# Optimization experiments

Hardware: AMD Instinct MI355X
Metric: run time of the kernel (lower is better)

The kernel has to match this reference:

```python
import jax, jax.numpy as jnp
import numpy as np

N_NODES = 50000
N_EDGES = 800000
IN_FEATS = 64
HID_FEATS = 64


def _sage_conv(x, src, dst, W_self, W_neigh, b):
    # mean aggregation over in-neighbors (messages flow src -> dst)
    msg_sum = jax.ops.segment_sum(x[src], dst, num_segments=N_NODES)  # [N, d]
    deg = jax.ops.segment_sum(jnp.ones((src.shape[0],), x.dtype), dst,
                              num_segments=N_NODES)  # [N]
    h_neigh = msg_sum / jnp.maximum(deg, 1.0)[:, None]  # zero-degree nodes -> 0
    return x @ W_self + h_neigh @ W_neigh + b


def setup_inputs() -> dict:
    key = jax.random.key(0)
    ks = jax.random.split(key, 12)
    inputs = jax.random.normal(ks[0], (N_NODES, IN_FEATS), dtype=jnp.float32)
    src = jax.random.randint(ks[1], (N_EDGES,), 0, N_NODES, dtype=jnp.int32)
    dst = jax.random.randint(ks[2], (N_EDGES,), 0, N_NODES, dtype=jnp.int32)

    def glorot(k, shape):
        lim = float(np.sqrt(6.0 / (shape[0] + shape[1])))
        return jax.random.uniform(k, shape, jnp.float32, -lim, lim)

    return {
        "inputs": inputs, "src": src, "dst": dst,
        "W_self1": glorot(ks[3], (IN_FEATS, HID_FEATS)),
        "W_neigh1": glorot(ks[4], (IN_FEATS, HID_FEATS)),
        "b1": jnp.zeros((HID_FEATS,), jnp.float32),
        "W_self2": glorot(ks[5], (HID_FEATS, HID_FEATS)),
        "W_neigh2": glorot(ks[6], (HID_FEATS, HID_FEATS)),
        "b2": jnp.zeros((HID_FEATS,), jnp.float32),
        "W_self3": glorot(ks[7], (HID_FEATS, 1)),
        "W_neigh3": glorot(ks[8], (HID_FEATS, 1)),
        "b3": jnp.zeros((1,), jnp.float32),
    }


def reference(inputs, src, dst,
              W_self1, W_neigh1, b1,
              W_self2, W_neigh2, b2,
              W_self3, W_neigh3, b3):
    h = jax.nn.relu(_sage_conv(inputs, src, dst, W_self1, W_neigh1, b1))
    h = jax.nn.relu(_sage_conv(h, src, dst, W_self2, W_neigh2, b2))
    h = _sage_conv(h, src, dst, W_self3, W_neigh3, b3)
    return h  # [N_NODES, 1]
```

## Files before the change

### kernel.cpp

```cpp
#include <hip/hip_runtime.h>

#define N_NODES 50000
#define N_EDGES 800000
#define F 64
#define NTILES (N_NODES / 16)

#define BNODES 128
#define NB ((N_NODES + BNODES - 1) / BNODES)
#define BCAP 2560
#define EPB 3200
#define SCAT_BLOCKS (N_EDGES / EPB)
#define PREP_ELEMS (4 * F * F + N_NODES * 16)
#define PREP_BLOCKS ((PREP_ELEMS + 511) / 512)

typedef __attribute__((ext_vector_type(8))) short short8;
typedef __attribute__((ext_vector_type(4))) float f32x4;

union frag16 { uint4 u; short8 s; };


__device__ __forceinline__ float bflo(unsigned int u) {
    union { unsigned int i; float f; } c; c.i = u << 16; return c.f;
}
__device__ __forceinline__ float bfhi(unsigned int u) {
    union { unsigned int i; float f; } c; c.i = u & 0xFFFF0000u; return c.f;
}
__device__ __forceinline__ unsigned short f2bf(float f) {
    union { float f; unsigned int i; } c; c.f = f;
    unsigned int r = c.i + 0x7FFF + ((c.i >> 16) & 1);
    return (unsigned short)(r >> 16);
}


__global__ __launch_bounds__(512) void scatter_prep(
        const int* __restrict__ src, const int* __restrict__ dst,
        int* __restrict__ bcur, unsigned int* __restrict__ binned,
        const float* __restrict__ W0, const float* __restrict__ W1,
        const float* __restrict__ W2, const float* __restrict__ W3,
        unsigned short* __restrict__ Wt,
        const float4* __restrict__ xin, ushort4* __restrict__ xout) {
    if (blockIdx.x >= SCAT_BLOCKS) {
        int idx = (blockIdx.x - SCAT_BLOCKS) * 512 + threadIdx.x;
        if (idx < 4 * F * F) {
            int m = idx >> 12;
            int e = idx & 4095;
            int n = e >> 6, k = e & 63;
            const float* W = (m == 0) ? W0 : (m == 1) ? W1 : (m == 2) ? W2 : W3;
            Wt[m * F * F + n * F + k] = f2bf(W[k * F + n]);
            return;
        }
        int i = idx - 4 * F * F;
        if (i >= N_NODES * 16) return;
        float4 v = xin[i];
        ushort4 o;
        o.x = f2bf(v.x); o.y = f2bf(v.y); o.z = f2bf(v.z); o.w = f2bf(v.w);
        xout[i] = o;
        return;
    }

    __shared__ int lcnt[NB];
    __shared__ int scan[512];
    __shared__ int gbase[NB];
    __shared__ int lcur[NB];
    __shared__ unsigned int staged[EPB];
    int tid = threadIdx.x;
    int e0 = blockIdx.x * EPB;
    int e1 = min(N_EDGES, e0 + EPB);
    for (int i = tid; i < NB; i += 512) lcnt[i] = 0;
    __syncthreads();
    for (int i = e0 + tid; i < e1; i += 512)
        atomicAdd(&lcnt[dst[i] >> 7], 1);
    __syncthreads();
    int v = (tid < NB) ? lcnt[tid] : 0;
    scan[tid] = v;
    __syncthreads();
    for (int off = 1; off < 512; off <<= 1) {
        int t = (tid >= off) ? scan[tid - off] : 0;
        __syncthreads();
        scan[tid] += t;
        __syncthreads();
    }
    if (tid < NB) {
        int excl = scan[tid] - v;
        int resv = (v > 0) ? atomicAdd(&bcur[tid], v) : 0;
        gbase[tid] = tid * BCAP + resv - excl;
        lcur[tid] = excl;
    }
    __syncthreads();
    for (int i = e0 + tid; i < e1; i += 512) {
        int d = dst[i];
        int b = d >> 7;
        int dl = d & 127;
        int posl = atomicAdd(&lcur[b], 1);
        staged[posl] = (unsigned)src[i] | ((unsigned)dl << 16) | ((unsigned)b << 23);
    }
    __syncthreads();
    int cnt = e1 - e0;
    for (int i = tid; i < cnt; i += 512) {
        unsigned pk = staged[i];
        int b = pk >> 23;
        binned[gbase[b] + i] = pk;
    }
}


__global__ __launch_bounds__(256) void bucket_build(const unsigned int* __restrict__ binned,
                                                    const int* __restrict__ bcur,
                                                    int* __restrict__ row_beg,
                                                    unsigned short* __restrict__ degs,
                                                    unsigned short* __restrict__ csr16) {
    int b = blockIdx.x;
    int start = b * BCAP;
    int cnt = bcur[b];
    __shared__ int ncnt[BNODES];
    __shared__ int nofs[BNODES];
    __shared__ int ncur[BNODES];
    int tid = threadIdx.x;
    for (int i = tid; i < BNODES; i += 256) ncnt[i] = 0;
    __syncthreads();
    for (int i = tid; i < cnt; i += 256)
        atomicAdd(&ncnt[(binned[start + i] >> 16) & 127], 1);
    __syncthreads();
    if (tid < 128) nofs[tid] = ncnt[tid];
    __syncthreads();
    for (int off = 1; off < 128; off <<= 1) {
        int t = (tid >= off && tid < 128) ? nofs[tid - off] : 0;
        __syncthreads();
        if (tid < 128) nofs[tid] += t;
        __syncthreads();
    }
    if (tid < 128) {
        int excl = nofs[tid] - ncnt[tid];
        ncur[tid] = excl;
        int node = b * BNODES + tid;
        row_beg[node] = start + excl;
        degs[node] = (unsigned short)ncnt[tid];
    }
    __syncthreads();
    for (int i = tid; i < cnt; i += 256) {
        unsigned pk = binned[start + i];
        int dl = (pk >> 16) & 127;
        int pos = start + atomicAdd(&ncur[dl], 1);
        csr16[pos] = (unsigned short)(pk & 0xFFFF);
    }
}


__global__ __launch_bounds__(256) void aggregate_kernel(
        const uint4* __restrict__ xh8, const int* __restrict__ row_beg,
        const unsigned short* __restrict__ degs,
        const unsigned short* __restrict__ csr16, uint4* __restrict__ aggh8, int n_nodes) {
    int wave = threadIdx.x >> 6;
    int lane = threadIdx.x & 63;
    int node = blockIdx.x * 4 + wave;
    if (node >= n_nodes) return;
    int g   = lane >> 3;
    int sub = lane & 7;
    int beg = row_beg[node];
    int deg = degs[node];
    int end = beg + deg;
    float a0[8], a1[8];
    #pragma unroll
    for (int j = 0; j < 8; ++j) { a0[j] = 0.f; a1[j] = 0.f; }
    int i = beg + g;
    for (; i + 8 < end; i += 16) {
        int i0 = csr16[i];
        int i1 = csr16[i + 8];
        uint4 v0 = xh8[i0 * 8 + sub];
        uint4 v1 = xh8[i1 * 8 + sub];
        a0[0] += bflo(v0.x); a0[1] += bfhi(v0.x); a0[2] += bflo(v0.y); a0[3] += bfhi(v0.y);
        a0[4] += bflo(v0.z); a0[5] += bfhi(v0.z); a0[6] += bflo(v0.w); a0[7] += bfhi(v0.w);
        a1[0] += bflo(v1.x); a1[1] += bfhi(v1.x); a1[2] += bflo(v1.y); a1[3] += bfhi(v1.y);
        a1[4] += bflo(v1.z); a1[5] += bfhi(v1.z); a1[6] += bflo(v1.w); a1[7] += bfhi(v1.w);
    }
    if (i < end) {
        uint4 v0 = xh8[csr16[i] * 8 + sub];
        a0[0] += bflo(v0.x); a0[1] += bfhi(v0.x); a0[2] += bflo(v0.y); a0[3] += bfhi(v0.y);
        a0[4] += bflo(v0.z); a0[5] += bfhi(v0.z); a0[6] += bflo(v0.w); a0[7] += bfhi(v0.w);
    }
    float s[8];
    #pragma unroll
    for (int j = 0; j < 8; ++j) s[j] = a0[j] + a1[j];
    #pragma unroll
    for (int off = 8; off <= 32; off <<= 1)
        #pragma unroll
        for (int j = 0; j < 8; ++j)
            s[j] += __shfl_xor(s[j], off);
    if (g == 0) {
        float inv = (deg > 0) ? (1.0f / (float)deg) : 0.f;
        unsigned short o[8];
        #pragma unroll
        for (int j = 0; j < 8; ++j) o[j] = f2bf(s[j] * inv);
        uint4 pk;
        pk.x = (unsigned)o[0] | ((unsigned)o[1] << 16);
        pk.y = (unsigned)o[2] | ((unsigned)o[3] << 16);
        pk.z = (unsigned)o[4] | ((unsigned)o[5] << 16);
        pk.w = (unsigned)o[6] | ((unsigned)o[7] << 16);
        aggh8[node * 8 + sub] = pk;
    }
}


__global__ __launch_bounds__(256) void mfma_transform(
        const uint4* __restrict__ xh, const uint4* __restrict__ aggh,
        const uint4* __restrict__ Wst, const uint4* __restrict__ Wnt,
        const float* __restrict__ b,
        unsigned short* __restrict__ out_bf,
        const float* __restrict__ Ws3, const float* __restrict__ Wn3,
        float* __restrict__ pout, float* __restrict__ qout, int ntiles) {
    int wv   = threadIdx.x >> 6;
    int lane = threadIdx.x & 63;
    int tile = blockIdx.x * 4 + wv;
    if (tile >= ntiles) return;
    int lo = lane & 15, hi = lane >> 4;

    frag16 ws[2][4], wn[2][4];
    #pragma unroll
    for (int kt = 0; kt < 2; ++kt)
        #pragma unroll
        for (int jt = 0; jt < 4; ++jt) {
            int n = jt * 16 + lo;
            ws[kt][jt].u = Wst[n * 8 + kt * 4 + hi];
            wn[kt][jt].u = Wnt[n * 8 + kt * 4 + hi];
        }

    float bias_s[4];
    #pragma unroll
    for (int jt = 0; jt < 4; ++jt) bias_s[jt] = b[jt * 16 + lo];
    float w3n_s[4], w3s_s[4];
    if (pout) {
        #pragma unroll
        for (int jt = 0; jt < 4; ++jt) {
            w3n_s[jt] = Wn3[jt * 16 + lo];
            w3s_s[jt] = Ws3[jt * 16 + lo];
        }
    }

    int base = tile * 16;
    int node = base + lo;

    frag16 ax[2], aa[2];
    #pragma unroll
    for (int kt = 0; kt < 2; ++kt) {
        ax[kt].u = xh[node * 8 + kt * 4 + hi];
        aa[kt].u = aggh[node * 8 + kt * 4 + hi];
    }

    f32x4 acc[4];
    #pragma unroll
    for (int jt = 0; jt < 4; ++jt)
        acc[jt] = f32x4{bias_s[jt], bias_s[jt], bias_s[jt], bias_s[jt]};

    #pragma unroll
    for (int kt = 0; kt < 2; ++kt)
        #pragma unroll
        for (int jt = 0; jt < 4; ++jt) {
            acc[jt] = __builtin_amdgcn_mfma_f32_16x16x32_bf16(ax[kt].s, ws[kt][jt].s, acc[jt], 0, 0, 0);
            acc[jt] = __builtin_amdgcn_mfma_f32_16x16x32_bf16(aa[kt].s, wn[kt][jt].s, acc[jt], 0, 0, 0);
        }

    if (out_bf) {
        #pragma unroll
        for (int jt = 0; jt < 4; ++jt)
            #pragma unroll
            for (int r = 0; r < 4; ++r) {
                float h = fmaxf(acc[jt][r], 0.f);
                out_bf[(base + hi * 4 + r) * F + jt * 16 + lo] = f2bf(h);
            }
    } else {
        #pragma unroll
        for (int r = 0; r < 4; ++r) {
            float pr = 0.f, qr = 0.f;
            #pragma unroll
            for (int jt = 0; jt < 4; ++jt) {
                float h = fmaxf(acc[jt][r], 0.f);
                pr += h * w3n_s[jt];
                qr += h * w3s_s[jt];
            }
            #pragma unroll
            for (int off = 1; off < 16; off <<= 1) {
                pr += __shfl_xor(pr, off);
                qr += __shfl_xor(qr, off);
            }
            if (lo == 0) {
                pout[base + hi * 4 + r] = pr;
                qout[base + hi * 4 + r] = qr;
            }
        }
    }
}


__global__ __launch_bounds__(256) void final_kernel(
        const int* __restrict__ row_beg, const unsigned short* __restrict__ degs,
        const unsigned short* __restrict__ csr16,
        const float* __restrict__ p, const float* __restrict__ q,
        const float* __restrict__ b3, float* __restrict__ out, int n_nodes) {
    int grp = threadIdx.x >> 4;
    int ln  = threadIdx.x & 15;
    int node = blockIdx.x * 16 + grp;
    if (node >= n_nodes) return;
    int beg = row_beg[node];
    int deg = degs[node];
    int end = beg + deg;
    float s = 0.f;
    for (int i = beg + ln; i < end; i += 16) s += p[csr16[i]];
    #pragma unroll
    for (int off = 1; off < 16; off <<= 1) s += __shfl_xor(s, off);
    if (ln == 0) {
        float inv = (deg > 0) ? (1.0f / (float)deg) : 0.f;
        out[node] = q[node] + s * inv + b3[0];
    }
}


extern "C" void kernel_launch(void* const* d_in, const int* in_sizes, int n_in,
                              void* d_out, int out_size, void* d_ws, size_t ws_size,
                              hipStream_t stream) {
    const float* x   = (const float*)d_in[0];
    const int*   src = (const int*)d_in[1];
    const int*   dst = (const int*)d_in[2];
    const float* Ws1 = (const float*)d_in[3];
    const float* Wn1 = (const float*)d_in[4];
    const float* b1  = (const float*)d_in[5];
    const float* Ws2 = (const float*)d_in[6];
    const float* Wn2 = (const float*)d_in[7];
    const float* b2  = (const float*)d_in[8];
    const float* Ws3 = (const float*)d_in[9];
    const float* Wn3 = (const float*)d_in[10];
    const float* b3  = (const float*)d_in[11];
    float* out = (float*)d_out;

    char* ws = (char*)d_ws;
    size_t cur = 0;
    auto alloc = [&](size_t bytes) -> void* {
        void* p = ws + cur;
        cur += (bytes + 255) & ~(size_t)255;
        return p;
    };

    int*            bcur     = (int*)  alloc(NB * sizeof(int));
    unsigned int*   binned   = (unsigned int*)alloc((size_t)NB * BCAP * sizeof(unsigned int));
    int*            row_beg  = (int*)  alloc((size_t)(NB * BNODES) * sizeof(int));
    unsigned short* degs     = (unsigned short*)alloc((size_t)(NB * BNODES) * sizeof(unsigned short));
    unsigned short* csr16    = (unsigned short*)alloc((size_t)NB * BCAP * sizeof(unsigned short));
    unsigned short* xh       = (unsigned short*)alloc((size_t)N_NODES * F * 2);
    unsigned short* h1h      = (unsigned short*)alloc((size_t)N_NODES * F * 2);
    unsigned short* aggh     = (unsigned short*)alloc((size_t)N_NODES * F * 2);
    unsigned short* Wt       = (unsigned short*)alloc(4 * F * F * 2);
    float*          p        = (float*)alloc(N_NODES * sizeof(float));
    float*          q        = (float*)alloc(N_NODES * sizeof(float));

    unsigned short* Wst1 = Wt;
    unsigned short* Wnt1 = Wt + F * F;
    unsigned short* Wst2 = Wt + 2 * F * F;
    unsigned short* Wnt2 = Wt + 3 * F * F;

    (void)hipMemsetAsync(bcur, 0, NB * sizeof(int), stream);
    scatter_prep<<<SCAT_BLOCKS + PREP_BLOCKS, 512, 0, stream>>>(
        src, dst, bcur, binned,
        Ws1, Wn1, Ws2, Wn2, Wt, (const float4*)x, (ushort4*)xh);
    bucket_build<<<NB, 256, 0, stream>>>(binned, bcur, row_beg, degs, csr16);

    int agg_grid = (N_NODES + 3) / 4;
    int tf_grid  = (NTILES + 3) / 4;

    aggregate_kernel<<<agg_grid, 256, 0, stream>>>(
        (const uint4*)xh, row_beg, degs, csr16, (uint4*)aggh, N_NODES);
    mfma_transform<<<tf_grid, 256, 0, stream>>>(
        (const uint4*)xh, (const uint4*)aggh, (const uint4*)Wst1, (const uint4*)Wnt1,
        b1, h1h, nullptr, nullptr, nullptr, nullptr, NTILES);
    aggregate_kernel<<<agg_grid, 256, 0, stream>>>(
        (const uint4*)h1h, row_beg, degs, csr16, (uint4*)aggh, N_NODES);
    mfma_transform<<<tf_grid, 256, 0, stream>>>(
        (const uint4*)h1h, (const uint4*)aggh, (const uint4*)Wst2, (const uint4*)Wnt2,
        b2, nullptr, Ws3, Wn3, p, q, NTILES);
    final_kernel<<<(N_NODES + 15) / 16, 256, 0, stream>>>(
        row_beg, degs, csr16, p, q, b3, out, N_NODES);
}
```

Baseline: 182.0 us.

## Fuse neighbor aggregation into MFMA transform and restructure edge scatter kernels

Merges the aggregate and MFMA transform kernels into one templated kernel: each block aggregates 16 nodes into shared memory, then one wave runs the MFMA tile. This removes the global aggh round trip and two launches. The scatter kernel now uses a fixed 512-block grid with grid-stride prep work and smaller edge chunks, and it keeps src/dst in registers instead of re-reading them. The bucket build uses 512 threads with register-held entries. The cost is that three of the four waves sit idle during the MFMA phase, and there are fewer blocks for the transform.

```diff
diff --git a/kernel.cpp b/kernel.cpp
--- a/kernel.cpp
+++ b/kernel.cpp
@@ -8,10 +8,11 @@
 #define BNODES 128
 #define NB ((N_NODES + BNODES - 1) / BNODES)
 #define BCAP 2560
-#define EPB 3200
-#define SCAT_BLOCKS (N_EDGES / EPB)
+#define EPB 2048
+#define SCHUNKS ((N_EDGES + EPB - 1) / EPB)
+#define SGRID 512
+#define SBLOCK 512
 #define PREP_ELEMS (4 * F * F + N_NODES * 16)
-#define PREP_BLOCKS ((PREP_ELEMS + 511) / 512)
 
 typedef __attribute__((ext_vector_type(8))) short short8;
 typedef __attribute__((ext_vector_type(4))) float f32x4;
@@ -32,52 +33,64 @@
 }
 
 
-__global__ __launch_bounds__(512) void scatter_prep(
+__global__ __launch_bounds__(SBLOCK) void scatter_prep(
         const int* __restrict__ src, const int* __restrict__ dst,
         int* __restrict__ bcur, unsigned int* __restrict__ binned,
         const float* __restrict__ W0, const float* __restrict__ W1,
         const float* __restrict__ W2, const float* __restrict__ W3,
         unsigned short* __restrict__ Wt,
         const float4* __restrict__ xin, ushort4* __restrict__ xout) {
-    if (blockIdx.x >= SCAT_BLOCKS) {
-        int idx = (blockIdx.x - SCAT_BLOCKS) * 512 + threadIdx.x;
+    __shared__ int lcnt[NB];
+    __shared__ int scan[SBLOCK];
+    __shared__ int gbase[NB];
+    __shared__ int lcur[NB];
+    __shared__ unsigned int staged[EPB];
+
+    int tid = threadIdx.x;
+    int blk = blockIdx.x;
+
+    for (int idx = blk * SBLOCK + tid; idx < PREP_ELEMS; idx += SGRID * SBLOCK) {
         if (idx < 4 * F * F) {
             int m = idx >> 12;
             int e = idx & 4095;
             int n = e >> 6, k = e & 63;
             const float* W = (m == 0) ? W0 : (m == 1) ? W1 : (m == 2) ? W2 : W3;
             Wt[m * F * F + n * F + k] = f2bf(W[k * F + n]);
-            return;
-        }
-        int i = idx - 4 * F * F;
-        if (i >= N_NODES * 16) return;
-        float4 v = xin[i];
-        ushort4 o;
-        o.x = f2bf(v.x); o.y = f2bf(v.y); o.z = f2bf(v.z); o.w = f2bf(v.w);
-        xout[i] = o;
-        return;
-    }
-
-    __shared__ int lcnt[NB];
-    __shared__ int scan[512];
-    __shared__ int gbase[NB];
-    __shared__ int lcur[NB];
-    __shared__ unsigned int staged[EPB];
-    int tid = threadIdx.x;
-    int e0 = blockIdx.x * EPB;
+        } else {
+            int i = idx - 4 * F * F;
+            float4 v = xin[i];
+            ushort4 o;
+            o.x = f2bf(v.x); o.y = f2bf(v.y); o.z = f2bf(v.z); o.w = f2bf(v.w);
+            xout[i] = o;
+        }
+    }
+
+    if (blk >= SCHUNKS) return;
+
+    int e0 = blk * EPB;
     int e1 = min(N_EDGES, e0 + EPB);
-    for (int i = tid; i < NB; i += 512) lcnt[i] = 0;
-    __syncthreads();
-    for (int i = e0 + tid; i < e1; i += 512)
-        atomicAdd(&lcnt[dst[i] >> 7], 1);
-    __syncthreads();
+    for (int i = tid; i < NB; i += SBLOCK) lcnt[i] = 0;
+    __syncthreads();
+
+    int dreg[4], sreg[4];
+    #pragma unroll
+    for (int t = 0; t < 4; ++t) {
+        int i = e0 + tid + t * SBLOCK;
+        if (i < e1) { dreg[t] = dst[i]; sreg[t] = src[i]; }
+        else        { dreg[t] = -1;     sreg[t] = 0; }
+    }
+    #pragma unroll
+    for (int t = 0; t < 4; ++t)
+        if (dreg[t] >= 0) atomicAdd(&lcnt[dreg[t] >> 7], 1);
+    __syncthreads();
+
     int v = (tid < NB) ? lcnt[tid] : 0;
     scan[tid] = v;
     __syncthreads();
-    for (int off = 1; off < 512; off <<= 1) {
-        int t = (tid >= off) ? scan[tid - off] : 0;
+    for (int off = 1; off < SBLOCK; off <<= 1) {
+        int t2 = (tid >= off) ? scan[tid - off] : 0;
         __syncthreads();
-        scan[tid] += t;
+        scan[tid] += t2;
         __syncthreads();
     }
     if (tid < NB) {
@@ -87,131 +100,151 @@
         lcur[tid] = excl;
     }
     __syncthreads();
-    for (int i = e0 + tid; i < e1; i += 512) {
-        int d = dst[i];
-        int b = d >> 7;
-        int dl = d & 127;
-        int posl = atomicAdd(&lcur[b], 1);
-        staged[posl] = (unsigned)src[i] | ((unsigned)dl << 16) | ((unsigned)b << 23);
-    }
-    __syncthreads();
+
+    #pragma unroll
+    for (int t = 0; t < 4; ++t) {
+        if (dreg[t] >= 0) {
+            int d = dreg[t];
+            int b = d >> 7;
+            int dl = d & 127;
+            int posl = atomicAdd(&lcur[b], 1);
+            staged[posl] = (unsigned)sreg[t] | ((unsigned)dl << 16) | ((unsigned)b << 23);
+        }
+    }
+    __syncthreads();
+
     int cnt = e1 - e0;
-    for (int i = tid; i < cnt; i += 512) {
+    for (int i = tid; i < cnt; i += SBLOCK) {
         unsigned pk = staged[i];
-        int b = pk >> 23;
-        binned[gbase[b] + i] = pk;
-    }
-}
-
-
-__global__ __launch_bounds__(256) void bucket_build(const unsigned int* __restrict__ binned,
-                                                    const int* __restrict__ bcur,
-                                                    int* __restrict__ row_beg,
-                                                    unsigned short* __restrict__ degs,
-                                                    unsigned short* __restrict__ csr16) {
-    int b = blockIdx.x;
-    int start = b * BCAP;
-    int cnt = bcur[b];
+        binned[gbase[pk >> 23] + i] = pk;
+    }
+}
+
+
+__global__ __launch_bounds__(512) void bucket_build(
+        const unsigned int* __restrict__ binned, const int* __restrict__ bcur,
+        int* __restrict__ row_beg, unsigned short* __restrict__ degs,
+        unsigned short* __restrict__ csr16) {
     __shared__ int ncnt[BNODES];
     __shared__ int nofs[BNODES];
     __shared__ int ncur[BNODES];
+    int blk = blockIdx.x;
     int tid = threadIdx.x;
-    for (int i = tid; i < BNODES; i += 256) ncnt[i] = 0;
-    __syncthreads();
-    for (int i = tid; i < cnt; i += 256)
-        atomicAdd(&ncnt[(binned[start + i] >> 16) & 127], 1);
-    __syncthreads();
-    if (tid < 128) nofs[tid] = ncnt[tid];
-    __syncthreads();
-    for (int off = 1; off < 128; off <<= 1) {
-        int t = (tid >= off && tid < 128) ? nofs[tid - off] : 0;
+    int start = blk * BCAP;
+    int cnt = min(bcur[blk], BCAP);
+
+    for (int i = tid; i < BNODES; i += 512) ncnt[i] = 0;
+    __syncthreads();
+
+    unsigned preg[5];
+    #pragma unroll
+    for (int t = 0; t < 5; ++t) {
+        int i = tid + t * 512;
+        preg[t] = (i < cnt) ? binned[start + i] : 0xFFFFFFFFu;
+    }
+    #pragma unroll
+    for (int t = 0; t < 5; ++t)
+        if (preg[t] != 0xFFFFFFFFu)
+            atomicAdd(&ncnt[(preg[t] >> 16) & 127], 1);
+    __syncthreads();
+
+    if (tid < BNODES) nofs[tid] = ncnt[tid];
+    __syncthreads();
+    for (int off = 1; off < BNODES; off <<= 1) {
+        int t2 = (tid >= off && tid < BNODES) ? nofs[tid - off] : 0;
         __syncthreads();
-        if (tid < 128) nofs[tid] += t;
+        if (tid < BNODES) nofs[tid] += t2;
         __syncthreads();
     }
-    if (tid < 128) {
+    if (tid < BNODES) {
         int excl = nofs[tid] - ncnt[tid];
         ncur[tid] = excl;
-        int node = b * BNODES + tid;
+        int node = blk * BNODES + tid;
         row_beg[node] = start + excl;
         degs[node] = (unsigned short)ncnt[tid];
     }
     __syncthreads();
-    for (int i = tid; i < cnt; i += 256) {
-        unsigned pk = binned[start + i];
-        int dl = (pk >> 16) & 127;
-        int pos = start + atomicAdd(&ncur[dl], 1);
-        csr16[pos] = (unsigned short)(pk & 0xFFFF);
-    }
-}
-
-
-__global__ __launch_bounds__(256) void aggregate_kernel(
+
+    #pragma unroll
+    for (int t = 0; t < 5; ++t) {
+        if (preg[t] != 0xFFFFFFFFu) {
+            unsigned pk = preg[t];
+            int dl = (pk >> 16) & 127;
+            int pos = start + atomicAdd(&ncur[dl], 1);
+            csr16[pos] = (unsigned short)(pk & 0xFFFF);
+        }
+    }
+}
+
+
+template <bool PROJ>
+__global__ __launch_bounds__(256) void aggtf_kernel(
         const uint4* __restrict__ xh8, const int* __restrict__ row_beg,
         const unsigned short* __restrict__ degs,
-        const unsigned short* __restrict__ csr16, uint4* __restrict__ aggh8, int n_nodes) {
-    int wave = threadIdx.x >> 6;
-    int lane = threadIdx.x & 63;
-    int node = blockIdx.x * 4 + wave;
-    if (node >= n_nodes) return;
+        const unsigned short* __restrict__ csr16,
+        const uint4* __restrict__ Wst, const uint4* __restrict__ Wnt,
+        const float* __restrict__ b, unsigned short* __restrict__ out_bf,
+        const float* __restrict__ Ws3, const float* __restrict__ Wn3,
+        float* __restrict__ pout, float* __restrict__ qout) {
+    __shared__ uint4 lagg[16 * 8];
+    int tid  = threadIdx.x;
+    int wave = tid >> 6;
+    int lane = tid & 63;
+    int base = blockIdx.x * 16;
+
     int g   = lane >> 3;
     int sub = lane & 7;
-    int beg = row_beg[node];
-    int deg = degs[node];
-    int end = beg + deg;
-    float a0[8], a1[8];
-    #pragma unroll
-    for (int j = 0; j < 8; ++j) { a0[j] = 0.f; a1[j] = 0.f; }
-    int i = beg + g;
-    for (; i + 8 < end; i += 16) {
-        int i0 = csr16[i];
-        int i1 = csr16[i + 8];
-        uint4 v0 = xh8[i0 * 8 + sub];
-        uint4 v1 = xh8[i1 * 8 + sub];
-        a0[0] += bflo(v0.x); a0[1] += bfhi(v0.x); a0[2] += bflo(v0.y); a0[3] += bfhi(v0.y);
-        a0[4] += bflo(v0.z); a0[5] += bfhi(v0.z); a0[6] += bflo(v0.w); a0[7] += bfhi(v0.w);
-        a1[0] += bflo(v1.x); a1[1] += bfhi(v1.x); a1[2] += bflo(v1.y); a1[3] += bfhi(v1.y);
-        a1[4] += bflo(v1.z); a1[5] += bfhi(v1.z); a1[6] += bflo(v1.w); a1[7] += bfhi(v1.w);
-    }
-    if (i < end) {
-        uint4 v0 = xh8[csr16[i] * 8 + sub];
-        a0[0] += bflo(v0.x); a0[1] += bfhi(v0.x); a0[2] += bflo(v0.y); a0[3] += bfhi(v0.y);
-        a0[4] += bflo(v0.z); a0[5] += bfhi(v0.z); a0[6] += bflo(v0.w); a0[7] += bfhi(v0.w);
-    }
-    float s[8];
-    #pragma unroll
-    for (int j = 0; j < 8; ++j) s[j] = a0[j] + a1[j];
-    #pragma unroll
-    for (int off = 8; off <= 32; off <<= 1)
-        #pragma unroll
-        for (int j = 0; j < 8; ++j)
-            s[j] += __shfl_xor(s[j], off);
-    if (g == 0) {
-        float inv = (deg > 0) ? (1.0f / (float)deg) : 0.f;
-        unsigned short o[8];
-        #pragma unroll
-        for (int j = 0; j < 8; ++j) o[j] = f2bf(s[j] * inv);
-        uint4 pk;
-        pk.x = (unsigned)o[0] | ((unsigned)o[1] << 16);
-        pk.y = (unsigned)o[2] | ((unsigned)o[3] << 16);
-        pk.z = (unsigned)o[4] | ((unsigned)o[5] << 16);
-        pk.w = (unsigned)o[6] | ((unsigned)o[7] << 16);
-        aggh8[node * 8 + sub] = pk;
-    }
-}
-
-
-__global__ __launch_bounds__(256) void mfma_transform(
-        const uint4* __restrict__ xh, const uint4* __restrict__ aggh,
-        const uint4* __restrict__ Wst, const uint4* __restrict__ Wnt,
-        const float* __restrict__ b,
-        unsigned short* __restrict__ out_bf,
-        const float* __restrict__ Ws3, const float* __restrict__ Wn3,
-        float* __restrict__ pout, float* __restrict__ qout, int ntiles) {
-    int wv   = threadIdx.x >> 6;
-    int lane = threadIdx.x & 63;
-    int tile = blockIdx.x * 4 + wv;
-    if (tile >= ntiles) return;
+
+    int rb_l = 0, dg_l = 0;
+    if (lane < 16) { rb_l = row_beg[base + lane]; dg_l = degs[base + lane]; }
+
+    for (int nl = wave * 4; nl < wave * 4 + 4; ++nl) {
+        int beg = __shfl(rb_l, nl);
+        int deg = __shfl(dg_l, nl);
+        int end = beg + deg;
+        float a0[8], a1[8];
+        #pragma unroll
+        for (int j = 0; j < 8; ++j) { a0[j] = 0.f; a1[j] = 0.f; }
+        int i = beg + g;
+        for (; i + 8 < end; i += 16) {
+            int i0 = csr16[i];
+            int i1 = csr16[i + 8];
+            uint4 v0 = xh8[i0 * 8 + sub];
+            uint4 v1 = xh8[i1 * 8 + sub];
+            a0[0] += bflo(v0.x); a0[1] += bfhi(v0.x); a0[2] += bflo(v0.y); a0[3] += bfhi(v0.y);
+            a0[4] += bflo(v0.z); a0[5] += bfhi(v0.z); a0[6] += bflo(v0.w); a0[7] += bfhi(v0.w);
+            a1[0] += bflo(v1.x); a1[1] += bfhi(v1.x); a1[2] += bflo(v1.y); a1[3] += bfhi(v1.y);
+            a1[4] += bflo(v1.z); a1[5] += bfhi(v1.z); a1[6] += bflo(v1.w); a1[7] += bfhi(v1.w);
+        }
+        if (i < end) {
+            uint4 v0 = xh8[csr16[i] * 8 + sub];
+            a0[0] += bflo(v0.x); a0[1] += bfhi(v0.x); a0[2] += bflo(v0.y); a0[3] += bfhi(v0.y);
+            a0[4] += bflo(v0.z); a0[5] += bfhi(v0.z); a0[6] += bflo(v0.w); a0[7] += bfhi(v0.w);
+        }
+        float s[8];
+        #pragma unroll
+        for (int j = 0; j < 8; ++j) s[j] = a0[j] + a1[j];
+        #pragma unroll
+        for (int off = 8; off <= 32; off <<= 1)
+            #pragma unroll
+            for (int j = 0; j < 8; ++j)
+                s[j] += __shfl_xor(s[j], off);
+        if (g == 0) {
+            float inv = (deg > 0) ? (1.0f / (float)deg) : 0.f;
+            unsigned short o[8];
+            #pragma unroll
+            for (int j = 0; j < 8; ++j) o[j] = f2bf(s[j] * inv);
+            uint4 pk;
+            pk.x = (unsigned)o[0] | ((unsigned)o[1] << 16);
+            pk.y = (unsigned)o[2] | ((unsigned)o[3] << 16);
+            pk.z = (unsigned)o[4] | ((unsigned)o[5] << 16);
+            pk.w = (unsigned)o[6] | ((unsigned)o[7] << 16);
+            lagg[nl * 8 + sub] = pk;
+        }
+    }
+    __syncthreads();
+    if (wave != 0) return;
+
     int lo = lane & 15, hi = lane >> 4;
 
     frag16 ws[2][4], wn[2][4];
@@ -223,12 +256,11 @@
             ws[kt][jt].u = Wst[n * 8 + kt * 4 + hi];
             wn[kt][jt].u = Wnt[n * 8 + kt * 4 + hi];
         }
-
     float bias_s[4];
     #pragma unroll
     for (int jt = 0; jt < 4; ++jt) bias_s[jt] = b[jt * 16 + lo];
     float w3n_s[4], w3s_s[4];
-    if (pout) {
+    if constexpr (PROJ) {
         #pragma unroll
         for (int jt = 0; jt < 4; ++jt) {
             w3n_s[jt] = Wn3[jt * 16 + lo];
@@ -236,14 +268,11 @@
         }
     }
 
-    int base = tile * 16;
-    int node = base + lo;
-
     frag16 ax[2], aa[2];
     #pragma unroll
     for (int kt = 0; kt < 2; ++kt) {
-        ax[kt].u = xh[node * 8 + kt * 4 + hi];
-        aa[kt].u = aggh[node * 8 + kt * 4 + hi];
+        ax[kt].u = xh8[(base + lo) * 8 + kt * 4 + hi];
+        aa[kt].u = lagg[lo * 8 + kt * 4 + hi];
     }
 
     f32x4 acc[4];
@@ -259,7 +288,7 @@
             acc[jt] = __builtin_amdgcn_mfma_f32_16x16x32_bf16(aa[kt].s, wn[kt][jt].s, acc[jt], 0, 0, 0);
         }
 
-    if (out_bf) {
+    if constexpr (!PROJ) {
         #pragma unroll
         for (int jt = 0; jt < 4; ++jt)
             #pragma unroll
@@ -334,9 +363,9 @@
     char* ws = (char*)d_ws;
     size_t cur = 0;
     auto alloc = [&](size_t bytes) -> void* {
-        void* p = ws + cur;
+        void* ptr = ws + cur;
         cur += (bytes + 255) & ~(size_t)255;
-        return p;
+        return ptr;
     };
 
     int*            bcur     = (int*)  alloc(NB * sizeof(int));
@@ -346,7 +375,6 @@
     unsigned short* csr16    = (unsigned short*)alloc((size_t)NB * BCAP * sizeof(unsigned short));
     unsigned short* xh       = (unsigned short*)alloc((size_t)N_NODES * F * 2);
     unsigned short* h1h      = (unsigned short*)alloc((size_t)N_NODES * F * 2);
-    unsigned short* aggh     = (unsigned short*)alloc((size_t)N_NODES * F * 2);
     unsigned short* Wt       = (unsigned short*)alloc(4 * F * F * 2);
     float*          p        = (float*)alloc(N_NODES * sizeof(float));
     float*          q        = (float*)alloc(N_NODES * sizeof(float));
@@ -357,24 +385,18 @@
     unsigned short* Wnt2 = Wt + 3 * F * F;
 
     (void)hipMemsetAsync(bcur, 0, NB * sizeof(int), stream);
-    scatter_prep<<<SCAT_BLOCKS + PREP_BLOCKS, 512, 0, stream>>>(
-        src, dst, bcur, binned,
-        Ws1, Wn1, Ws2, Wn2, Wt, (const float4*)x, (ushort4*)xh);
-    bucket_build<<<NB, 256, 0, stream>>>(binned, bcur, row_beg, degs, csr16);
-
-    int agg_grid = (N_NODES + 3) / 4;
-    int tf_grid  = (NTILES + 3) / 4;
-
-    aggregate_kernel<<<agg_grid, 256, 0, stream>>>(
-        (const uint4*)xh, row_beg, degs, csr16, (uint4*)aggh, N_NODES);
-    mfma_transform<<<tf_grid, 256, 0, stream>>>(
-        (const uint4*)xh, (const uint4*)aggh, (const uint4*)Wst1, (const uint4*)Wnt1,
-        b1, h1h, nullptr, nullptr, nullptr, nullptr, NTILES);
-    aggregate_kernel<<<agg_grid, 256, 0, stream>>>(
-        (const uint4*)h1h, row_beg, degs, csr16, (uint4*)aggh, N_NODES);
-    mfma_transform<<<tf_grid, 256, 0, stream>>>(
-        (const uint4*)h1h, (const uint4*)aggh, (const uint4*)Wst2, (const uint4*)Wnt2,
-        b2, nullptr, Ws3, Wn3, p, q, NTILES);
+    scatter_prep<<<SGRID, SBLOCK, 0, stream>>>(
+        src, dst, bcur, binned, Ws1, Wn1, Ws2, Wn2, Wt, (const float4*)x, (ushort4*)xh);
+    bucket_build<<<NB, 512, 0, stream>>>(binned, bcur, row_beg, degs, csr16);
+
+    aggtf_kernel<false><<<NTILES, 256, 0, stream>>>(
+        (const uint4*)xh, row_beg, degs, csr16,
+        (const uint4*)Wst1, (const uint4*)Wnt1, b1, h1h,
+        nullptr, nullptr, nullptr, nullptr);
+    aggtf_kernel<true><<<NTILES, 256, 0, stream>>>(
+        (const uint4*)h1h, row_beg, degs, csr16,
+        (const uint4*)Wst2, (const uint4*)Wnt2, b2, nullptr,
+        Ws3, Wn3, p, q);
     final_kernel<<<(N_NODES + 15) / 16, 256, 0, stream>>>(
         row_beg, degs, csr16, p, q, b3, out, N_NODES);
 }
```

Result: faster. 167.9 us (-7.7%).
